# Kernel optimization log

Hardware: AMD Instinct MI355X
Metric: run time of the kernel (lower is better)

The kernel has to match this reference:

```python
import jax, jax.numpy as jnp
import numpy as np
from math import sqrt

B, S, D, H = 4, 2048, 1024, 16
DH = D // H          # 64
DF = 4 * D           # 4096
EPS = 1e-5
NEG = -1e9


def layer_norm(x, w, b):
    mu = jnp.mean(x, axis=-1, keepdims=True)
    var = jnp.mean((x - mu) ** 2, axis=-1, keepdims=True)
    return (x - mu) * jax.lax.rsqrt(var + EPS) * w + b


def setup_inputs() -> dict:
    key = jax.random.key(0)
    ks = jax.random.split(key, 16)
    s = 0.02
    return {
        "state": jax.random.normal(ks[0], (B, S, D), jnp.float32),
        "mask": jax.random.randint(ks[1], (B, S), 0, 2, jnp.int32),
        "ln1_w": jnp.ones((D,), jnp.float32),
        "ln1_b": jnp.zeros((D,), jnp.float32),
        "Wq": jax.random.normal(ks[2], (H, D, DH), jnp.float32) * s,
        "bq": jnp.zeros((H, DH), jnp.float32),
        "Wk": jax.random.normal(ks[3], (H, D, DH), jnp.float32) * s,
        "bk": jnp.zeros((H, DH), jnp.float32),
        "Wv": jax.random.normal(ks[4], (H, D, DH), jnp.float32) * s,
        "bv": jnp.zeros((H, DH), jnp.float32),
        "Wo": jax.random.normal(ks[5], (D, D), jnp.float32) * s,
        "bo": jnp.zeros((D,), jnp.float32),
        "ln2_w": jnp.ones((D,), jnp.float32),
        "ln2_b": jnp.zeros((D,), jnp.float32),
        "W1": jax.random.normal(ks[6], (D, DF), jnp.float32) * s,
        "b1": jnp.zeros((DF,), jnp.float32),
        "W2": jax.random.normal(ks[7], (DF, D), jnp.float32) * s,
        "b2": jnp.zeros((D,), jnp.float32),
    }


def reference(state, mask, ln1_w, ln1_b, Wq, bq, Wk, bk, Wv, bv, Wo, bo,
              ln2_w, ln2_b, W1, b1, W2, b2):
    # pre-norm attention block
    hidden = layer_norm(state, ln1_w, ln1_b)               # [B,S,D]
    q = jnp.einsum("bsd,hde->bhse", hidden, Wq) + bq[None, :, None, :]
    k = jnp.einsum("bsd,hde->bhse", hidden, Wk) + bk[None, :, None, :]
    v = jnp.einsum("bsd,hde->bhse", hidden, Wv) + bv[None, :, None, :]
    scores = jnp.einsum("bhse,bhte->bhst", q, k) / sqrt(DH)  # [B,H,S,S]
    scores = jnp.where(mask[:, None, None, :] == 0, NEG, scores)
    weights = jax.nn.softmax(scores, axis=-1)
    attended = jnp.einsum("bhst,bhte->bhse", weights, v)    # [B,H,S,DH]
    # concat heads in head order (matches torch cat over per-head outputs)
    attended = attended.transpose(0, 2, 1, 3).reshape(B, S, D)
    attn_out = attended @ Wo + bo
    output = state + attn_out
    # pre-norm FFN block (dropout=0 -> identity)
    hidden = layer_norm(output, ln2_w, ln2_b)
    ff = jax.nn.gelu(hidden @ W1 + b1, approximate=False) @ W2 + b2
    return output + ff
```

## Files before the change

kernel.cpp:

```cpp
#include <hip/hip_runtime.h>
#include <math.h>

#define B_  4
#define S_  2048
#define D_  1024
#define H_  16
#define DH_ 64
#define DF_ 4096
#define M_  8192

#define QSC 0.18033688011112042f

typedef __attribute__((ext_vector_type(8))) short bf8_t;
typedef __attribute__((ext_vector_type(4))) float f4_t;

#if defined(__has_builtin)
#if __has_builtin(__builtin_amdgcn_cvt_pk_bf16_f32)
#define HAVE_PKCVT 1
#endif
#if __has_builtin(__builtin_amdgcn_global_load_lds)
#define HAVE_ASYNC 1
#endif
#if __has_builtin(__builtin_amdgcn_exp2f)
#define EXP2F(x) __builtin_amdgcn_exp2f(x)
#else
#define EXP2F(x) __expf((x) * 0.69314718055994531f)
#endif
#else
#define EXP2F(x) __expf((x) * 0.69314718055994531f)
#endif

__device__ __forceinline__ unsigned pk_bf16(float lo, float hi) {
#ifdef HAVE_PKCVT
  auto r = __builtin_amdgcn_cvt_pk_bf16_f32(lo, hi);
  unsigned u; __builtin_memcpy(&u, &r, 4); return u;
#else
  union { float f; unsigned u; } a, b2; a.f = lo; b2.f = hi;
  unsigned ra = a.u + 0x7fffu + ((a.u >> 16) & 1u);
  unsigned rb = b2.u + 0x7fffu + ((b2.u >> 16) & 1u);
  return (ra >> 16) | (rb & 0xffff0000u);
#endif
}

__device__ __forceinline__ unsigned short f2bf(float x) {
  return (unsigned short)(pk_bf16(x, x) & 0xffffu);
}

__device__ __forceinline__ bf8_t upk8(unsigned u0, unsigned u1, unsigned u2, unsigned u3) {
  union { unsigned u[4]; bf8_t v; } c;
  c.u[0] = u0; c.u[1] = u1; c.u[2] = u2; c.u[3] = u3; return c.v;
}

__device__ __forceinline__ f4_t mfma32(bf8_t a, bf8_t b, f4_t c) {
  return __builtin_amdgcn_mfma_f32_16x16x32_bf16(a, b, c, 0, 0, 0);
}

__device__ __forceinline__ void async16(const void* g, void* l) {
#ifdef HAVE_ASYNC
  __builtin_amdgcn_global_load_lds((__attribute__((address_space(1))) void*)(g),
                                   (__attribute__((address_space(3))) void*)(l), 16, 0, 0);
#else
  *(uint4*)l = *(const uint4*)g;
#endif
}

__device__ __forceinline__ int sw(int row) { return (row ^ (row >> 3)) & 7; }


__global__ __launch_bounds__(256) void wtrans_kernel(const float* __restrict__ in,
                                                     unsigned short* __restrict__ out,
                                                     int K, int N) {
  const int k0 = blockIdx.x * 32, n0 = blockIdx.y * 32;
  __shared__ float t[32][33];
  const int tid = threadIdx.x;
#pragma unroll
  for (int i = 0; i < 4; i++) {
    int idx = i * 256 + tid; int r = idx >> 5, c = idx & 31;
    t[r][c] = in[(size_t)(k0 + r) * N + n0 + c];
  }
  __syncthreads();
#pragma unroll
  for (int i = 0; i < 4; i++) {
    int idx = i * 256 + tid; int r = idx >> 5, c = idx & 31;
    out[(size_t)(n0 + r) * K + k0 + c] = f2bf(t[c][r]);
  }
}

__global__ __launch_bounds__(256) void qkvpack_kernel(const float* __restrict__ Wq,
                                                      const float* __restrict__ Wk,
                                                      const float* __restrict__ Wv,
                                                      unsigned short* __restrict__ WqkvT) {
  const int z = blockIdx.z;
  const int sel = z >> 4, h = z & 15;
  const float* in = (sel == 0 ? Wq : sel == 1 ? Wk : Wv) + (size_t)h * D_ * DH_;
  const int k0 = blockIdx.x * 32, n0 = blockIdx.y * 32;
  __shared__ float t[32][33];
  const int tid = threadIdx.x;
#pragma unroll
  for (int i = 0; i < 4; i++) {
    int idx = i * 256 + tid; int r = idx >> 5, c = idx & 31;
    t[r][c] = in[(size_t)(k0 + r) * DH_ + n0 + c];
  }
  __syncthreads();
#pragma unroll
  for (int i = 0; i < 4; i++) {
    int idx = i * 256 + tid; int r = idx >> 5, c = idx & 31;
    int n = sel * 1024 + h * 64 + n0 + r;
    WqkvT[(size_t)n * D_ + k0 + c] = f2bf(t[c][r]);
  }
}

__global__ void biaspack_kernel(const float* __restrict__ bq, const float* __restrict__ bk,
                                const float* __restrict__ bv, float* __restrict__ bqkv) {
  int i = blockIdx.x * 256 + threadIdx.x;
  if (i < 3072) {
    int sel = i >> 10, j = i & 1023;
    const float* src = sel == 0 ? bq : sel == 1 ? bk : bv;
    bqkv[i] = src[j];
  }
}


__global__ __launch_bounds__(256) void ln_kernel(const float* __restrict__ x,
                                                 const float* __restrict__ w,
                                                 const float* __restrict__ bb,
                                                 unsigned short* __restrict__ out) {
  const int row = blockIdx.x;
  const float* xr = x + (size_t)row * D_;
  const int tid = threadIdx.x;
  float v[4]; float s = 0.f;
#pragma unroll
  for (int i = 0; i < 4; i++) { v[i] = xr[tid + i * 256]; s += v[i]; }
  __shared__ float red[8];
#pragma unroll
  for (int o = 32; o; o >>= 1) s += __shfl_xor(s, o, 64);
  const int wv = tid >> 6, ln = tid & 63;
  if (!ln) red[wv] = s;
  __syncthreads();
  float mean = (red[0] + red[1] + red[2] + red[3]) * (1.f / 1024.f);
  float s2 = 0.f;
#pragma unroll
  for (int i = 0; i < 4; i++) { float d = v[i] - mean; s2 += d * d; }
#pragma unroll
  for (int o = 32; o; o >>= 1) s2 += __shfl_xor(s2, o, 64);
  if (!ln) red[4 + wv] = s2;
  __syncthreads();
  float var = (red[4] + red[5] + red[6] + red[7]) * (1.f / 1024.f);
  float rstd = rsqrtf(var + 1e-5f);
#pragma unroll
  for (int i = 0; i < 4; i++) {
    int c = tid + i * 256;
    out[(size_t)row * D_ + c] = f2bf((v[i] - mean) * rstd * w[c] + bb[c]);
  }
}

template <int EPI>
__global__ __launch_bounds__(256) void gemm_bt(const unsigned short* __restrict__ A,
                                               const unsigned short* __restrict__ Bt,
                                               const float* __restrict__ bias,
                                               const float* __restrict__ resid,
                                               unsigned short* __restrict__ outb,
                                               float* __restrict__ outf,
                                               unsigned short* __restrict__ vTout,
                                               int Ndim, int Kdim) {
  __shared__ __align__(16) unsigned short Asmem[4096];
  __shared__ __align__(16) unsigned short Bsmem[4096];
  const int tid = threadIdx.x;
  const int wave = tid >> 6, lane = tid & 63;
  const int quad = lane >> 4, l16 = lane & 15;
  const int wm = wave >> 1, wn = wave & 1;
  const int m0 = blockIdx.y * 128, n0 = blockIdx.x * 128;

  const f4_t fzero = {0.f, 0.f, 0.f, 0.f};
  f4_t acc[4][4];
#pragma unroll
  for (int i = 0; i < 4; i++)
#pragma unroll
    for (int j = 0; j < 4; j++) acc[i][j] = fzero;

  const int rowA = tid >> 2;
  const int kp = (tid & 3) * 8;

  for (int k0 = 0; k0 < Kdim; k0 += 32) {
    __syncthreads();
#pragma unroll
    for (int r = 0; r < 2; r++) {
      const int row = r * 64 + rowA;
      const int e = row * 32 + kp;
      async16(A  + (size_t)(m0 + row) * Kdim + k0 + kp, &Asmem[e]);
      async16(Bt + (size_t)(n0 + row) * Kdim + k0 + kp, &Bsmem[e]);
    }
    __syncthreads();

    bf8_t a[4], b[4];
#pragma unroll
    for (int i = 0; i < 4; i++) {
      a[i] = *(const bf8_t*)&Asmem[(wm * 64 + i * 16 + l16) * 32 + quad * 8];
      b[i] = *(const bf8_t*)&Bsmem[(wn * 64 + i * 16 + l16) * 32 + quad * 8];
    }
#pragma unroll
    for (int i = 0; i < 4; i++)
#pragma unroll
      for (int j = 0; j < 4; j++)
        acc[i][j] = mfma32(a[i], b[j], acc[i][j]);
  }

  if (EPI == 0 && n0 >= 2048) {
    const int bb2 = m0 >> 11;
    const int s_base = (m0 & 2047) + wm * 64;
#pragma unroll
    for (int i = 0; i < 4; i++) {
      const int g0 = (i & 2) * 16 + 8 * quad + 4 * (i & 1);
#pragma unroll
      for (int j = 0; j < 4; j++) {
        const int n = n0 + wn * 64 + j * 16 + l16;
        const int ef = n - 2048;
        const int hh = ef >> 6, e = ef & 63;
        const float bsv = bias[n];
        uint2 wq;
        wq.x = pk_bf16(acc[i][j][0] + bsv, acc[i][j][1] + bsv);
        wq.y = pk_bf16(acc[i][j][2] + bsv, acc[i][j][3] + bsv);
        *(uint2*)&vTout[(size_t)((bb2 * 16 + hh) * 64 + e) * S_ + s_base + g0] = wq;
      }
    }
    return;
  }

  const float sc = (EPI == 0 && n0 < 1024) ? QSC : 1.f;
#pragma unroll
  for (int i = 0; i < 4; i++) {
#pragma unroll
    for (int j = 0; j < 4; j++) {
#pragma unroll
      for (int r = 0; r < 4; r++) {
        const int m = m0 + wm * 64 + i * 16 + quad * 4 + r;
        const int n = n0 + wn * 64 + j * 16 + l16;
        float v = acc[i][j][r] + bias[n];
        if constexpr (EPI == 0) v *= sc;
        if constexpr (EPI == 2) v = 0.5f * v * (1.f + erff(v * 0.70710678118654752f));
        if constexpr (EPI == 1) {
          v += resid[(size_t)m * Ndim + n];
          outf[(size_t)m * Ndim + n] = v;
        } else {
          outb[(size_t)m * Ndim + n] = f2bf(v);
        }
      }
    }
  }
}


__global__ __launch_bounds__(256) void attn_kernel(const unsigned short* __restrict__ qkv,
                                                   const unsigned short* __restrict__ vT,
                                                   const int* __restrict__ maskp,
                                                   unsigned short* __restrict__ attended) {
  const int bh = blockIdx.y, b = bh >> 4, h = bh & 15;
  const int q0 = blockIdx.x * 128;
  const int tid = threadIdx.x, wv = tid >> 6, lane = tid & 63;
  const int quad = lane >> 4, l16 = lane & 15;
  __shared__ __align__(16) unsigned short smem[16384];
  __shared__ float biasl[128];
  unsigned short* Ks = smem;
  unsigned short* Vs = smem + 8192;

  bf8_t aq[2][2];
#pragma unroll
  for (int sb = 0; sb < 2; sb++) {
    const unsigned short* qrow =
        qkv + (size_t)(b * S_ + q0 + wv * 32 + sb * 16 + l16) * 3072 + h * 64;
    aq[sb][0] = *(const bf8_t*)(qrow + quad * 8);
    aq[sb][1] = *(const bf8_t*)(qrow + 32 + quad * 8);
  }

  const bf8_t ones8 = {0x3F80, 0x3F80, 0x3F80, 0x3F80, 0x3F80, 0x3F80, 0x3F80, 0x3F80};
  const f4_t fzero = {0.f, 0.f, 0.f, 0.f};
  f4_t o[2][4], lacc[2];
#pragma unroll
  for (int sb = 0; sb < 2; sb++) {
    lacc[sb] = fzero;
#pragma unroll
    for (int ee = 0; ee < 4; ee++) o[sb][ee] = fzero;
  }

  for (int t0 = 0; t0 < S_; t0 += 128) {
    __syncthreads();
#pragma unroll
    for (int r = 0; r < 4; r++) {
      int ci = r * 256 + tid;
      int krow = ci >> 3, kc = (ci & 7) ^ sw(krow);
      async16(qkv + (size_t)(b * S_ + t0 + krow) * 3072 + 1024 + h * 64 + kc * 8,
              &Ks[ci * 8]);
      int e = ci >> 4, half = (ci >> 3) & 1, vc = (ci & 7) ^ sw(e);
      async16(vT + (size_t)(bh * 64 + e) * S_ + t0 + half * 64 + vc * 8,
              &Vs[ci * 8]);
    }
    if (tid < 128) biasl[tid] = maskp[b * S_ + t0 + tid] ? 0.f : -8e9f;
    __syncthreads();

#pragma unroll
    for (int th = 0; th < 2; th++) {
      f4_t sf[2][4];
#pragma unroll
      for (int jj = 0; jj < 4; jj++) {
        f4_t bi = *(const f4_t*)&biasl[th * 64 + jj * 16 + quad * 4];
        sf[0][jj] = bi;
        sf[1][jj] = bi;
      }
#pragma unroll
      for (int jj = 0; jj < 4; jj++) {
        int krow = th * 64 + jj * 16 + l16, sk = sw(krow);
        bf8_t kf0 = *(const bf8_t*)&Ks[krow * 64 + (quad ^ sk) * 8];
        bf8_t kf1 = *(const bf8_t*)&Ks[krow * 64 + ((quad + 4) ^ sk) * 8];
        sf[0][jj] = mfma32(kf0, aq[0][0], sf[0][jj]);
        sf[0][jj] = mfma32(kf1, aq[0][1], sf[0][jj]);
        sf[1][jj] = mfma32(kf0, aq[1][0], sf[1][jj]);
        sf[1][jj] = mfma32(kf1, aq[1][1], sf[1][jj]);
      }

      bf8_t pp[2][2];
#pragma unroll
      for (int sb = 0; sb < 2; sb++) {
#pragma unroll
        for (int h2 = 0; h2 < 2; h2++) {
          float p0 = EXP2F(sf[sb][2 * h2][0]),     p1 = EXP2F(sf[sb][2 * h2][1]);
          float p2 = EXP2F(sf[sb][2 * h2][2]),     p3 = EXP2F(sf[sb][2 * h2][3]);
          float p4 = EXP2F(sf[sb][2 * h2 + 1][0]), p5 = EXP2F(sf[sb][2 * h2 + 1][1]);
          float p6 = EXP2F(sf[sb][2 * h2 + 1][2]), p7 = EXP2F(sf[sb][2 * h2 + 1][3]);
          pp[sb][h2] = upk8(pk_bf16(p0, p1), pk_bf16(p2, p3),
                            pk_bf16(p4, p5), pk_bf16(p6, p7));
        }
        lacc[sb] = mfma32(ones8, pp[sb][0], lacc[sb]);
        lacc[sb] = mfma32(ones8, pp[sb][1], lacc[sb]);
      }

#pragma unroll
      for (int ee = 0; ee < 4; ee++) {
        int vrow = ee * 16 + l16, sv = sw(vrow);
#pragma unroll
        for (int h2 = 0; h2 < 2; h2++) {
          bf8_t vf = *(const bf8_t*)&Vs[vrow * 128 + th * 64 + ((4 * h2 + quad) ^ sv) * 8];
          o[0][ee] = mfma32(vf, pp[0][h2], o[0][ee]);
          o[1][ee] = mfma32(vf, pp[1][h2], o[1][ee]);
        }
      }
    }
  }

  float linv[2];
#pragma unroll
  for (int sb = 0; sb < 2; sb++) linv[sb] = 1.f / lacc[sb][0];

  __syncthreads();
  unsigned short* Os = smem;
#pragma unroll
  for (int sb = 0; sb < 2; sb++) {
    int srow = wv * 32 + sb * 16 + l16;
#pragma unroll
    for (int ee = 0; ee < 4; ee++) {
      unsigned w0 = pk_bf16(o[sb][ee][0] * linv[sb], o[sb][ee][1] * linv[sb]);
      unsigned w1 = pk_bf16(o[sb][ee][2] * linv[sb], o[sb][ee][3] * linv[sb]);
      uint2 wq; wq.x = w0; wq.y = w1;
      *(uint2*)&Os[srow * 72 + ee * 16 + quad * 4] = wq;
    }
  }
  __syncthreads();
#pragma unroll
  for (int it = 0; it < 4; it++) {
    int row = it * 32 + (tid >> 3), e0 = (tid & 7) * 8;
    bf8_t v = *(const bf8_t*)&Os[row * 72 + e0];
    *(bf8_t*)&attended[(size_t)(b * S_ + q0 + row) * D_ + h * 64 + e0] = v;
  }
}


extern "C" void kernel_launch(void* const* d_in, const int* in_sizes, int n_in,
                              void* d_out, int out_size, void* d_ws, size_t ws_size,
                              hipStream_t stream) {
  const float* state = (const float*)d_in[0];
  const int*   maskp = (const int*)d_in[1];
  const float* ln1w  = (const float*)d_in[2];
  const float* ln1b  = (const float*)d_in[3];
  const float* Wq    = (const float*)d_in[4];
  const float* bq    = (const float*)d_in[5];
  const float* Wk    = (const float*)d_in[6];
  const float* bk    = (const float*)d_in[7];
  const float* Wv    = (const float*)d_in[8];
  const float* bv    = (const float*)d_in[9];
  const float* Wo    = (const float*)d_in[10];
  const float* bo    = (const float*)d_in[11];
  const float* ln2w  = (const float*)d_in[12];
  const float* ln2b  = (const float*)d_in[13];
  const float* W1    = (const float*)d_in[14];
  const float* b1    = (const float*)d_in[15];
  const float* W2    = (const float*)d_in[16];
  const float* b2    = (const float*)d_in[17];

  char* w = (char*)d_ws;
  unsigned short* hidden = (unsigned short*)w; w += (size_t)M_ * D_ * 2;
  unsigned short* qkv    = (unsigned short*)w; w += (size_t)M_ * 3072 * 2;
  unsigned short* vT     = (unsigned short*)w; w += (size_t)M_ * D_ * 2;
  float*          outp   = (float*)w;          w += (size_t)M_ * D_ * 4;
  unsigned short* WqkvT  = (unsigned short*)w; w += (size_t)3072 * D_ * 2;
  unsigned short* WoT    = (unsigned short*)w; w += (size_t)D_ * D_ * 2;
  unsigned short* W1T    = (unsigned short*)w; w += (size_t)DF_ * D_ * 2;
  unsigned short* W2T    = (unsigned short*)w; w += (size_t)D_ * DF_ * 2;
  float*          bqkv   = (float*)w;          w += 3072 * 4;
  unsigned short* ff1    = qkv;

  qkvpack_kernel<<<dim3(32, 2, 48), 256, 0, stream>>>(Wq, Wk, Wv, WqkvT);
  wtrans_kernel<<<dim3(32, 32), 256, 0, stream>>>(Wo, WoT, D_, D_);
  wtrans_kernel<<<dim3(32, 128), 256, 0, stream>>>(W1, W1T, D_, DF_);
  wtrans_kernel<<<dim3(128, 32), 256, 0, stream>>>(W2, W2T, DF_, D_);
  biaspack_kernel<<<12, 256, 0, stream>>>(bq, bk, bv, bqkv);

  ln_kernel<<<M_, 256, 0, stream>>>(state, ln1w, ln1b, hidden);
  gemm_bt<0><<<dim3(3072 / 128, M_ / 128), 256, 0, stream>>>(hidden, WqkvT, bqkv, nullptr,
                                                             qkv, nullptr, vT, 3072, D_);
  attn_kernel<<<dim3(S_ / 128, B_ * H_), 256, 0, stream>>>(qkv, vT, maskp, hidden);
  gemm_bt<1><<<dim3(D_ / 128, M_ / 128), 256, 0, stream>>>(hidden, WoT, bo, state,
                                                           nullptr, outp, nullptr, D_, D_);
  ln_kernel<<<M_, 256, 0, stream>>>(outp, ln2w, ln2b, hidden);
  gemm_bt<2><<<dim3(DF_ / 128, M_ / 128), 256, 0, stream>>>(hidden, W1T, b1, nullptr,
                                                            ff1, nullptr, nullptr, DF_, D_);
  gemm_bt<1><<<dim3(D_ / 128, M_ / 128), 256, 0, stream>>>(ff1, W2T, b2, outp,
                                                           nullptr, (float*)d_out, nullptr, D_, DF_);
}
```

Before: 612.9 us.

## Replace 128x128 GEMM with double-buffered 256x256 tile kernel using swizzled LDS

Swaps the simple 128x128, K=32, single-buffered GEMM for a 256x256, K=64 kernel with 8 waves. It double-buffers LDS with async global-to-LDS loads, XOR-swizzles the LDS layout to avoid bank conflicts, interleaves MFMA quarters with prefetch of the tile two steps ahead, uses s_setprio, and remaps workgroups across the grid for L2 locality. The aim is more reuse per loaded byte and overlap of memory traffic with matrix-core work in all four projection GEMMs. In exchange it uses 128 KB of LDS and many more accumulator registers, and the larger tiles give fewer workgroups (e.g. 128 for the Wo and W2 GEMMs), which may hurt occupancy and load balance.

```diff
diff --git a/kernel.cpp b/kernel.cpp
--- a/kernel.cpp
+++ b/kernel.cpp
@@ -155,72 +155,177 @@
 }
 
 template <int EPI>
-__global__ __launch_bounds__(256) void gemm_bt(const unsigned short* __restrict__ A,
-                                               const unsigned short* __restrict__ Bt,
-                                               const float* __restrict__ bias,
-                                               const float* __restrict__ resid,
-                                               unsigned short* __restrict__ outb,
-                                               float* __restrict__ outf,
-                                               unsigned short* __restrict__ vTout,
-                                               int Ndim, int Kdim) {
-  __shared__ __align__(16) unsigned short Asmem[4096];
-  __shared__ __align__(16) unsigned short Bsmem[4096];
+__global__ __launch_bounds__(512, 2) void gemm256(const unsigned short* __restrict__ A,
+                                                  const unsigned short* __restrict__ Bt,
+                                                  const float* __restrict__ bias,
+                                                  const float* __restrict__ resid,
+                                                  unsigned short* __restrict__ outb,
+                                                  float* __restrict__ outf,
+                                                  unsigned short* __restrict__ vTout,
+                                                  int Ndim, int Kdim) {
+  __shared__ __align__(16) unsigned short Asm2[2][16384];
+  __shared__ __align__(16) unsigned short Bsm2[2][16384];
   const int tid = threadIdx.x;
   const int wave = tid >> 6, lane = tid & 63;
   const int quad = lane >> 4, l16 = lane & 15;
-  const int wm = wave >> 1, wn = wave & 1;
-  const int m0 = blockIdx.y * 128, n0 = blockIdx.x * 128;
+  const int wm = wave >> 2, wn = wave & 3;
+
+  const int gx = gridDim.x;
+  const int nwg = gx * (int)gridDim.y;
+  const int lin = (int)blockIdx.y * gx + (int)blockIdx.x;
+  const int swz = (lin & 7) * (nwg >> 3) + (lin >> 3);
+  const int m0 = (swz / gx) * 256, n0 = (swz % gx) * 256;
+
+  const int NT = Kdim >> 6;
+  const unsigned short* Agb = A + (size_t)m0 * Kdim;
+  const unsigned short* Bgb = Bt + (size_t)n0 * Kdim;
+
+  const int srow = lane >> 3, schk = lane & 7;
+
+  auto stage8 = [&](const unsigned short* G, unsigned short* L, int row0) {
+    const int r = row0 + srow;
+    async16(G + (size_t)r * Kdim + ((schk ^ sw(r)) << 3), L + (row0 << 6));
+  };
+  auto stageA0 = [&](int t) {
+    const unsigned short* G = Agb + t * 64; unsigned short* L = Asm2[t & 1];
+    stage8(G, L, wave * 8); stage8(G, L, 128 + wave * 8);
+  };
+  auto stageA1 = [&](int t) {
+    const unsigned short* G = Agb + t * 64; unsigned short* L = Asm2[t & 1];
+    stage8(G, L, 64 + wave * 8); stage8(G, L, 192 + wave * 8);
+  };
+  auto stageB0 = [&](int t) {
+    const unsigned short* G = Bgb + t * 64; unsigned short* L = Bsm2[t & 1];
+    const int r0 = (wave >> 1) * 64 + (wave & 1) * 8;
+    stage8(G, L, r0); stage8(G, L, r0 + 16);
+  };
+  auto stageB1 = [&](int t) {
+    const unsigned short* G = Bgb + t * 64; unsigned short* L = Bsm2[t & 1];
+    const int r0 = (wave >> 1) * 64 + 32 + (wave & 1) * 8;
+    stage8(G, L, r0); stage8(G, L, r0 + 16);
+  };
+
+  auto frag = [&](const unsigned short* buf, int row, int s) -> bf8_t {
+    return *(const bf8_t*)&buf[(row << 6) + ((((s << 2) + quad) ^ sw(row)) << 3)];
+  };
 
   const f4_t fzero = {0.f, 0.f, 0.f, 0.f};
-  f4_t acc[4][4];
-#pragma unroll
-  for (int i = 0; i < 4; i++)
+  f4_t acc[8][4];
+#pragma unroll
+  for (int i = 0; i < 8; i++)
 #pragma unroll
     for (int j = 0; j < 4; j++) acc[i][j] = fzero;
 
-  const int rowA = tid >> 2;
-  const int kp = (tid & 3) * 8;
-
-  for (int k0 = 0; k0 < Kdim; k0 += 32) {
-    __syncthreads();
-#pragma unroll
-    for (int r = 0; r < 2; r++) {
-      const int row = r * 64 + rowA;
-      const int e = row * 32 + kp;
-      async16(A  + (size_t)(m0 + row) * Kdim + k0 + kp, &Asmem[e]);
-      async16(Bt + (size_t)(n0 + row) * Kdim + k0 + kp, &Bsmem[e]);
-    }
-    __syncthreads();
-
-    bf8_t a[4], b[4];
+  stageA0(0); stageA1(0); stageB0(0); stageB1(0);
+  stageA0(1); stageA1(1); stageB0(1); stageB1(1);
+  asm volatile("s_waitcnt vmcnt(8)" ::: "memory");
+  __builtin_amdgcn_s_barrier();
+
+  const int ar0 = wm << 7;
+  const int br0 = wn << 6;
+
+  for (int t = 0; t < NT; ++t) {
+    const unsigned short* Ab = Asm2[t & 1];
+    const unsigned short* Bb = Bsm2[t & 1];
+    const bool pf = (t + 2) < NT;
+    const int t2 = t + 2;
+    bf8_t af[4][2], bf0[2][2], bf1[2][2];
+
 #pragma unroll
     for (int i = 0; i < 4; i++) {
-      a[i] = *(const bf8_t*)&Asmem[(wm * 64 + i * 16 + l16) * 32 + quad * 8];
-      b[i] = *(const bf8_t*)&Bsmem[(wn * 64 + i * 16 + l16) * 32 + quad * 8];
-    }
-#pragma unroll
-    for (int i = 0; i < 4; i++)
-#pragma unroll
-      for (int j = 0; j < 4; j++)
-        acc[i][j] = mfma32(a[i], b[j], acc[i][j]);
+      af[i][0] = frag(Ab, ar0 + i * 16 + l16, 0);
+      af[i][1] = frag(Ab, ar0 + i * 16 + l16, 1);
+    }
+#pragma unroll
+    for (int j = 0; j < 2; j++) {
+      bf0[j][0] = frag(Bb, br0 + j * 16 + l16, 0);
+      bf0[j][1] = frag(Bb, br0 + j * 16 + l16, 1);
+    }
+    __builtin_amdgcn_s_barrier();
+    asm volatile("s_waitcnt lgkmcnt(0)" ::: "memory");
+    __builtin_amdgcn_s_setprio(1);
+#pragma unroll
+    for (int s = 0; s < 2; s++)
+#pragma unroll
+      for (int i = 0; i < 4; i++)
+#pragma unroll
+        for (int j = 0; j < 2; j++)
+          acc[i][j] = mfma32(af[i][s], bf0[j][s], acc[i][j]);
+    __builtin_amdgcn_s_setprio(0);
+    __builtin_amdgcn_s_barrier();
+
+#pragma unroll
+    for (int j = 0; j < 2; j++) {
+      bf1[j][0] = frag(Bb, br0 + 32 + j * 16 + l16, 0);
+      bf1[j][1] = frag(Bb, br0 + 32 + j * 16 + l16, 1);
+    }
+    if (pf) { stageA0(t2); stageB0(t2); }
+    __builtin_amdgcn_s_barrier();
+    asm volatile("s_waitcnt lgkmcnt(0)" ::: "memory");
+    __builtin_amdgcn_s_setprio(1);
+#pragma unroll
+    for (int s = 0; s < 2; s++)
+#pragma unroll
+      for (int i = 0; i < 4; i++)
+#pragma unroll
+        for (int j = 0; j < 2; j++)
+          acc[i][2 + j] = mfma32(af[i][s], bf1[j][s], acc[i][2 + j]);
+    __builtin_amdgcn_s_setprio(0);
+    __builtin_amdgcn_s_barrier();
+
+#pragma unroll
+    for (int i = 0; i < 4; i++) {
+      af[i][0] = frag(Ab, ar0 + 64 + i * 16 + l16, 0);
+      af[i][1] = frag(Ab, ar0 + 64 + i * 16 + l16, 1);
+    }
+    if (pf) stageB1(t2);
+    __builtin_amdgcn_s_barrier();
+    asm volatile("s_waitcnt lgkmcnt(0)" ::: "memory");
+    __builtin_amdgcn_s_setprio(1);
+#pragma unroll
+    for (int s = 0; s < 2; s++)
+#pragma unroll
+      for (int i = 0; i < 4; i++)
+#pragma unroll
+        for (int j = 0; j < 2; j++)
+          acc[4 + i][2 + j] = mfma32(af[i][s], bf1[j][s], acc[4 + i][2 + j]);
+    __builtin_amdgcn_s_setprio(0);
+    __builtin_amdgcn_s_barrier();
+
+    if (pf) stageA1(t2);
+    __builtin_amdgcn_s_barrier();
+    __builtin_amdgcn_s_setprio(1);
+#pragma unroll
+    for (int s = 0; s < 2; s++)
+#pragma unroll
+      for (int i = 0; i < 4; i++)
+#pragma unroll
+        for (int j = 0; j < 2; j++)
+          acc[4 + i][j] = mfma32(af[i][s], bf0[j][s], acc[4 + i][j]);
+    __builtin_amdgcn_s_setprio(0);
+    if (pf) asm volatile("s_waitcnt vmcnt(8)" ::: "memory");
+    else    asm volatile("s_waitcnt vmcnt(0)" ::: "memory");
+    __builtin_amdgcn_s_barrier();
   }
 
   if (EPI == 0 && n0 >= 2048) {
     const int bb2 = m0 >> 11;
-    const int s_base = (m0 & 2047) + wm * 64;
-#pragma unroll
-    for (int i = 0; i < 4; i++) {
-      const int g0 = (i & 2) * 16 + 8 * quad + 4 * (i & 1);
-#pragma unroll
-      for (int j = 0; j < 4; j++) {
-        const int n = n0 + wn * 64 + j * 16 + l16;
+    const int sb64 = (m0 & 2047) + (wm << 7);
+#pragma unroll
+    for (int mi = 0; mi < 8; mi++) {
+      const int i4 = mi & 3;
+      const int g0 = (i4 & 2) * 16 + 8 * quad + 4 * (i4 & 1);
+      const int sbase = sb64 + (mi >> 2) * 64 + g0;
+#pragma unroll
+      for (int nj = 0; nj < 4; nj++) {
+        const int n = n0 + wn * 64 + nj * 16 + l16;
         const int ef = n - 2048;
         const int hh = ef >> 6, e = ef & 63;
         const float bsv = bias[n];
         uint2 wq;
-        wq.x = pk_bf16(acc[i][j][0] + bsv, acc[i][j][1] + bsv);
-        wq.y = pk_bf16(acc[i][j][2] + bsv, acc[i][j][3] + bsv);
-        *(uint2*)&vTout[(size_t)((bb2 * 16 + hh) * 64 + e) * S_ + s_base + g0] = wq;
+        wq.x = pk_bf16(acc[mi][nj][0] + bsv, acc[mi][nj][1] + bsv);
+        wq.y = pk_bf16(acc[mi][nj][2] + bsv, acc[mi][nj][3] + bsv);
+        *(uint2*)&vTout[(size_t)((bb2 * 16 + hh) * 64 + e) * S_ + sbase] = wq;
       }
     }
     return;
@@ -228,14 +333,14 @@
 
   const float sc = (EPI == 0 && n0 < 1024) ? QSC : 1.f;
 #pragma unroll
-  for (int i = 0; i < 4; i++) {
-#pragma unroll
-    for (int j = 0; j < 4; j++) {
+  for (int mi = 0; mi < 8; mi++) {
+#pragma unroll
+    for (int nj = 0; nj < 4; nj++) {
 #pragma unroll
       for (int r = 0; r < 4; r++) {
-        const int m = m0 + wm * 64 + i * 16 + quad * 4 + r;
-        const int n = n0 + wn * 64 + j * 16 + l16;
-        float v = acc[i][j][r] + bias[n];
+        const int m = m0 + wm * 128 + mi * 16 + quad * 4 + r;
+        const int n = n0 + wn * 64 + nj * 16 + l16;
+        float v = acc[mi][nj][r] + bias[n];
         if constexpr (EPI == 0) v *= sc;
         if constexpr (EPI == 2) v = 0.5f * v * (1.f + erff(v * 0.70710678118654752f));
         if constexpr (EPI == 1) {
@@ -414,14 +519,14 @@
   biaspack_kernel<<<12, 256, 0, stream>>>(bq, bk, bv, bqkv);
 
   ln_kernel<<<M_, 256, 0, stream>>>(state, ln1w, ln1b, hidden);
-  gemm_bt<0><<<dim3(3072 / 128, M_ / 128), 256, 0, stream>>>(hidden, WqkvT, bqkv, nullptr,
+  gemm256<0><<<dim3(3072 / 256, M_ / 256), 512, 0, stream>>>(hidden, WqkvT, bqkv, nullptr,
                                                              qkv, nullptr, vT, 3072, D_);
   attn_kernel<<<dim3(S_ / 128, B_ * H_), 256, 0, stream>>>(qkv, vT, maskp, hidden);
-  gemm_bt<1><<<dim3(D_ / 128, M_ / 128), 256, 0, stream>>>(hidden, WoT, bo, state,
+  gemm256<1><<<dim3(D_ / 256, M_ / 256), 512, 0, stream>>>(hidden, WoT, bo, state,
                                                            nullptr, outp, nullptr, D_, D_);
   ln_kernel<<<M_, 256, 0, stream>>>(outp, ln2w, ln2b, hidden);
-  gemm_bt<2><<<dim3(DF_ / 128, M_ / 128), 256, 0, stream>>>(hidden, W1T, b1, nullptr,
+  gemm256<2><<<dim3(DF_ / 256, M_ / 256), 512, 0, stream>>>(hidden, W1T, b1, nullptr,
                                                             ff1, nullptr, nullptr, DF_, D_);
-  gemm_bt<1><<<dim3(D_ / 128, M_ / 128), 256, 0, stream>>>(ff1, W2T, b2, outp,
+  gemm256<1><<<dim3(D_ / 256, M_ / 256), 512, 0, stream>>>(ff1, W2T, b2, outp,
                                                            nullptr, (float*)d_out, nullptr, D_, DF_);
 }
```

Result: slower. 700.5 us (+14.3%).
